# Kernel optimization log

Measured on AMD Instinct MI355X. Metric: run time of the kernel, lower is better.

## Reference

```python
import jax, jax.numpy as jnp
import numpy as np
from jax import lax


def setup_inputs() -> dict:
    key = jax.random.key(0)
    ks = jax.random.split(key, 6)
    B, L, Cin, N, Cout = 4, 4096, 256, 512, 256
    s = 0.02
    return {
        "x": jax.random.normal(ks[0], (B, L, Cin), dtype=jnp.float32),
        "Wx": jax.random.normal(ks[1], (Cin, N), dtype=jnp.float32) * s,
        "bx": jnp.zeros((N,), dtype=jnp.float32),
        "Wbc": jax.random.normal(ks[2], (Cin, 2 * N), dtype=jnp.float32) * s,
        "bbc": jnp.zeros((2 * N,), dtype=jnp.float32),
        "Wd": jax.random.normal(ks[3], (Cin, N), dtype=jnp.float32) * s,
        "bd": jnp.zeros((N,), dtype=jnp.float32),
        "Wy": jax.random.normal(ks[4], (N, Cout), dtype=jnp.float32) * s,
        "by": jnp.zeros((Cout,), dtype=jnp.float32),
    }


def _scan_combine(c1, c2):
    # linear recurrence h_t = a_t * h_{t-1} + b_t as an associative op
    a1, b1 = c1
    a2, b2 = c2
    return a1 * a2, a2 * b1 + b2


def reference(x, Wx, bx, Wbc, bbc, Wd, bd, Wy, by):
    # projections: [B, L, N]
    x_proj = x @ Wx + bx
    BC = x @ Wbc + bbc
    delta = x @ Wd + bd
    Bm, C = jnp.split(BC, 2, axis=-1)

    A_bar = jnp.exp(-jax.nn.softplus(delta))      # [B, L, N], in (0, 1)
    B_bar = (1.0 - A_bar) * Bm                    # [B, L, N]

    # selective scan (h0 = 0): h_t = A_bar_t * h_{t-1} + B_bar_t * x_proj_t
    u = B_bar * x_proj
    _, h = lax.associative_scan(_scan_combine, (A_bar, u), axis=1)

    y = C * h                                      # [B, L, N]
    return y @ Wy + by                             # [B, L, Cout]
```

## Files before the change

kernel.cpp:

```cpp
#include <hip/hip_runtime.h>
#include <math.h>

constexpr int CIN  = 256;
constexpr int NST  = 512;
constexpr int LSEQ = 4096;
constexpr int BB   = 4;
constexpr int ROWS = BB * LSEQ;
constexpr int COUT = 256;
constexpr int LC   = 32;
constexpr int NC   = LSEQ / LC;

typedef __attribute__((ext_vector_type(8))) short bf16x8;
typedef __attribute__((ext_vector_type(4))) float f32x4;
typedef unsigned short ushort_t;
typedef unsigned int   uint_t;

__device__ __forceinline__ ushort_t f2bf(float f) {
    uint_t u = __float_as_uint(f);
    u = (u + 0x7FFF + ((u >> 16) & 1)) >> 16;
    return (ushort_t)u;
}
__device__ __forceinline__ float bf2f(ushort_t s) {
    return __uint_as_float(((uint_t)s) << 16);
}

constexpr int WELEMS  = 4 * NST * CIN + COUT * NST;
constexpr int WBLOCKS = WELEMS / 256;
constexpr int XBLOCKS = (ROWS * CIN / 4) / 256;

__global__ __launch_bounds__(256)
void prep_kernel(const float* __restrict__ Wx, const float* __restrict__ Wbc,
                 const float* __restrict__ Wd, const float* __restrict__ Wy,
                 const float* __restrict__ x,
                 ushort_t* __restrict__ Wt, ushort_t* __restrict__ Wyt,
                 ushort_t* __restrict__ xb)
{
    const int bid = blockIdx.x;
    if (bid < WBLOCKS) {
        const int gid = bid * 256 + threadIdx.x;
        if (gid < 4 * NST * CIN) {
            const int mat = gid >> 17;
            const int idx = gid & 131071;
            const int k   = idx >> 9;
            const int n   = idx & 511;
            float v;
            if      (mat == 0) v = Wx [k * NST + n];
            else if (mat == 1) v = Wbc[k * (2 * NST) + n];
            else if (mat == 2) v = Wbc[k * (2 * NST) + NST + n];
            else               v = Wd [k * NST + n];
            Wt[((size_t)mat * NST + n) * CIN + k] = f2bf(v);
        } else {
            const int idx = gid - 4 * NST * CIN;
            const int k   = idx >> 8;
            const int n   = idx & 255;
            Wyt[(size_t)n * NST + k] = f2bf(Wy[k * COUT + n]);
        }
    } else {
        const int i = ((bid - WBLOCKS) * 256 + threadIdx.x) * 4;
        float4 v = *(const float4*)&x[i];
        uint2 o;
        o.x = (uint_t)f2bf(v.x) | ((uint_t)f2bf(v.y) << 16);
        o.y = (uint_t)f2bf(v.z) | ((uint_t)f2bf(v.w) << 16);
        *(uint2*)&xb[i] = o;
    }
}

__global__ __launch_bounds__(256, 3)
void proj_mfma_kernel(const ushort_t* __restrict__ xb, const ushort_t* __restrict__ Wt,
                      const float* __restrict__ bx, const float* __restrict__ bbc,
                      const float* __restrict__ bd,
                      float2* __restrict__ AU, ushort_t* __restrict__ CYb,
                      float* __restrict__ Aprod, float* __restrict__ Hend)
{
    __shared__ alignas(16) char smem[46080];
    ushort_t (*xs)[72]     = (ushort_t(*)[72])smem;
    ushort_t (*ws)[64][72] = (ushort_t(*)[64][72])(smem + 9216);
    float2   (*aus)[65]    = (float2(*)[65])smem;
    float2   (*comb)[64]   = (float2(*)[64])(smem + 33280);

    const int tid  = threadIdx.x;
    const int wave = tid >> 6;
    const int lane = tid & 63;
    const int lm   = lane & 15;
    const int lq   = lane >> 4;
    const int row0 = blockIdx.x * 64;
    const int n0   = blockIdx.y * 64;

    const int sr = tid >> 2;
    const int sk = (tid & 3) << 4;

    f32x4 acc[4][4];
    #pragma unroll
    for (int rt = 0; rt < 4; ++rt)
        #pragma unroll
        for (int m = 0; m < 4; ++m)
            acc[rt][m] = (f32x4){0.f, 0.f, 0.f, 0.f};

    const ushort_t* xsrc  = xb + (size_t)(row0 + sr) * CIN + sk;
    const ushort_t* wsrc0 = Wt + (size_t)(n0 + sr) * CIN + sk;

    for (int k0 = 0; k0 < CIN; k0 += 64) {
        uint4 xv0 = *(const uint4*)(xsrc + k0);
        uint4 xv1 = *(const uint4*)(xsrc + k0 + 8);
        uint4 wv[4][2];
        #pragma unroll
        for (int m = 0; m < 4; ++m) {
            const ushort_t* p = wsrc0 + (size_t)m * NST * CIN + k0;
            wv[m][0] = *(const uint4*)(p);
            wv[m][1] = *(const uint4*)(p + 8);
        }
        *(uint4*)&xs[sr][sk]     = xv0;
        *(uint4*)&xs[sr][sk + 8] = xv1;
        #pragma unroll
        for (int m = 0; m < 4; ++m) {
            *(uint4*)&ws[m][sr][sk]     = wv[m][0];
            *(uint4*)&ws[m][sr][sk + 8] = wv[m][1];
        }
        __syncthreads();

        #pragma unroll
        for (int ks = 0; ks < 2; ++ks) {
            const int kk = ks * 32 + lq * 8;
            bf16x8 af[4], bf[4];
            #pragma unroll
            for (int rt = 0; rt < 4; ++rt)
                af[rt] = *(const bf16x8*)&xs[rt * 16 + lm][kk];
            #pragma unroll
            for (int m = 0; m < 4; ++m)
                bf[m] = *(const bf16x8*)&ws[m][wave * 16 + lm][kk];
            #pragma unroll
            for (int rt = 0; rt < 4; ++rt)
                #pragma unroll
                for (int m = 0; m < 4; ++m)
                    acc[rt][m] = __builtin_amdgcn_mfma_f32_16x16x32_bf16(
                        af[rt], bf[m], acc[rt][m], 0, 0, 0);
        }
        __syncthreads();
    }

    const int nl = wave * 16 + lm;
    const int ng = n0 + nl;
    const float bxv = bx [ng];
    const float bbv = bbc[ng];
    const float bcv = bbc[NST + ng];
    const float bdv = bd [ng];
    #pragma unroll
    for (int rt = 0; rt < 4; ++rt) {
        #pragma unroll
        for (int r = 0; r < 4; ++r) {
            const int t   = rt * 16 + lq * 4 + r;
            const int row = row0 + t;
            float xp = acc[rt][0][r] + bxv;
            float bm = acc[rt][1][r] + bbv;
            float cc = acc[rt][2][r] + bcv;
            float dd = acc[rt][3][r] + bdv;
            dd = fminf(dd, 60.0f);
            float e  = __expf(dd);
            float A  = 1.0f / (1.0f + e);
            float u  = (e * A) * bm * xp;
            const size_t idx = (size_t)row * NST + ng;
            AU[idx]  = make_float2(A, u);
            CYb[idx] = f2bf(cc);
            aus[t][nl] = make_float2(A, u);
        }
    }
    __syncthreads();

    {
        const int n  = tid & 63;
        const int sg = tid >> 6;
        float ap = 1.0f, h = 0.0f;
        #pragma unroll
        for (int i = 0; i < 16; ++i) {
            float2 au = aus[sg * 16 + i][n];
            ap *= au.x;
            h  = fmaf(au.x, h, au.y);
        }
        comb[sg][n] = make_float2(ap, h);
    }
    __syncthreads();

    if (tid < 128) {
        const int n  = tid & 63;
        const int ch = tid >> 6;
        float2 c0 = comb[ch * 2 + 0][n];
        float2 c1 = comb[ch * 2 + 1][n];
        const size_t ci = (size_t)(blockIdx.x * 2 + ch) * NST + (n0 + n);
        Aprod[ci] = c0.x * c1.x;
        Hend[ci]  = fmaf(c1.x, c0.y, c1.y);
    }
}

__global__ __launch_bounds__(256)
void scan_carry_kernel(const float* __restrict__ Aprod, const float* __restrict__ Hend,
                       float* __restrict__ Carry)
{
    const int gid = blockIdx.x * 256 + threadIdx.x;
    const int n   = gid & (NST - 1);
    const int b   = gid >> 9;
    float h = 0.0f;
    for (int c = 0; c < NC; ++c) {
        size_t idx = ((size_t)(b * NC + c)) * NST + n;
        Carry[idx] = h;
        h = fmaf(Aprod[idx], h, Hend[idx]);
    }
}

__global__ __launch_bounds__(256)
void scan_final_kernel(const float2* __restrict__ AU, ushort_t* __restrict__ CYb,
                       const float* __restrict__ Carry)
{
    const int gid = blockIdx.x * 256 + threadIdx.x;
    const int n   = gid & (NST - 1);
    const int bc  = gid >> 9;
    const size_t base = (size_t)bc * LC * NST + n;
    float h = Carry[(size_t)bc * NST + n];
    #pragma unroll 8
    for (int t = 0; t < LC; ++t) {
        size_t idx = base + (size_t)t * NST;
        float2 au = AU[idx];
        float cc  = bf2f(CYb[idx]);
        h = fmaf(au.x, h, au.y);
        CYb[idx] = f2bf(cc * h);
    }
}

__global__ __launch_bounds__(256, 4)
void out_mfma_kernel(const ushort_t* __restrict__ yb, const ushort_t* __restrict__ Wyt,
                     const float* __restrict__ by, float* __restrict__ out)
{
    __shared__ alignas(16) ushort_t ys [64][72];
    __shared__ alignas(16) ushort_t wys[64][72];

    const int tid  = threadIdx.x;
    const int wave = tid >> 6;
    const int lane = tid & 63;
    const int lm   = lane & 15;
    const int lq   = lane >> 4;
    const int row0 = blockIdx.x * 64;
    const int n0   = blockIdx.y * 64;

    const int sr = tid >> 2;
    const int sk = (tid & 3) << 4;

    f32x4 acc[4];
    #pragma unroll
    for (int rt = 0; rt < 4; ++rt) acc[rt] = (f32x4){0.f, 0.f, 0.f, 0.f};

    const ushort_t* ysrc = yb  + (size_t)(row0 + sr) * NST + sk;
    const ushort_t* wsrc = Wyt + (size_t)(n0  + sr) * NST + sk;

    for (int k0 = 0; k0 < NST; k0 += 64) {
        uint4 yv0 = *(const uint4*)(ysrc + k0);
        uint4 yv1 = *(const uint4*)(ysrc + k0 + 8);
        uint4 wv0 = *(const uint4*)(wsrc + k0);
        uint4 wv1 = *(const uint4*)(wsrc + k0 + 8);
        *(uint4*)&ys [sr][sk]     = yv0;
        *(uint4*)&ys [sr][sk + 8] = yv1;
        *(uint4*)&wys[sr][sk]     = wv0;
        *(uint4*)&wys[sr][sk + 8] = wv1;
        __syncthreads();

        #pragma unroll
        for (int ks = 0; ks < 2; ++ks) {
            const int kk = ks * 32 + lq * 8;
            bf16x8 bfr = *(const bf16x8*)&wys[wave * 16 + lm][kk];
            #pragma unroll
            for (int rt = 0; rt < 4; ++rt) {
                bf16x8 af = *(const bf16x8*)&ys[rt * 16 + lm][kk];
                acc[rt] = __builtin_amdgcn_mfma_f32_16x16x32_bf16(
                    af, bfr, acc[rt], 0, 0, 0);
            }
        }
        __syncthreads();
    }

    const int ng = n0 + wave * 16 + lm;
    const float bv = by[ng];
    #pragma unroll
    for (int rt = 0; rt < 4; ++rt)
        #pragma unroll
        for (int r = 0; r < 4; ++r) {
            const int row = row0 + rt * 16 + lq * 4 + r;
            out[(size_t)row * COUT + ng] = acc[rt][r] + bv;
        }
}

extern "C" void kernel_launch(void* const* d_in, const int* in_sizes, int n_in,
                              void* d_out, int out_size, void* d_ws, size_t ws_size,
                              hipStream_t stream)
{
    const float* x   = (const float*)d_in[0];
    const float* Wx  = (const float*)d_in[1];
    const float* bx  = (const float*)d_in[2];
    const float* Wbc = (const float*)d_in[3];
    const float* bbc = (const float*)d_in[4];
    const float* Wd  = (const float*)d_in[5];
    const float* bd  = (const float*)d_in[6];
    const float* Wy  = (const float*)d_in[7];
    const float* by  = (const float*)d_in[8];
    float* out = (float*)d_out;

    char* p = (char*)d_ws;
    float2*   AU    = (float2*)p;         p += (size_t)ROWS * NST * 8;
    ushort_t* CYb   = (ushort_t*)p;       p += (size_t)ROWS * NST * 2;
    ushort_t* xb    = (ushort_t*)p;       p += (size_t)ROWS * CIN * 2;
    ushort_t* Wt    = (ushort_t*)p;       p += (size_t)4 * NST * CIN * 2;
    ushort_t* Wyt   = (ushort_t*)p;       p += (size_t)COUT * NST * 2;
    float*    Aprod = (float*)p;          p += (size_t)BB * NC * NST * 4;
    float*    Hend  = (float*)p;          p += (size_t)BB * NC * NST * 4;
    float*    Carry = (float*)p;          p += (size_t)BB * NC * NST * 4;

    prep_kernel<<<WBLOCKS + XBLOCKS, 256, 0, stream>>>(
        Wx, Wbc, Wd, Wy, x, Wt, Wyt, xb);

    proj_mfma_kernel<<<dim3(ROWS / 64, NST / 64), 256, 0, stream>>>(
        xb, Wt, bx, bbc, bd, AU, CYb, Aprod, Hend);

    scan_carry_kernel<<<(BB * NST) / 256, 256, 0, stream>>>(
        Aprod, Hend, Carry);

    scan_final_kernel<<<(BB * NC * NST) / 256, 256, 0, stream>>>(
        AU, CYb, Carry);

    out_mfma_kernel<<<dim3(ROWS / 64, COUT / 64), 256, 0, stream>>>(
        CYb, Wyt, by, out);
}
```

Before: 162.7 us.

## Store scan A/u as fp16, coalesce C stores, parallelize carry scan across waves

Packs the per-element decay A and input u into one half2 word written with nontemporal stores, halving the intermediate AU traffic between the projection and final scan kernels. The bf16 C values are staged in shared memory and written out as 16-byte vector stores. The chunk aggregates are merged into one float2 array. The serial carry loop over chunks is replaced by a wave-level shuffle scan, one wavefront per (batch, state) pair. The fp16 storage of A and u lowers precision of the recurrence inputs and may hurt accuracy for long sequences.

```diff
diff --git a/kernel.cpp b/kernel.cpp
--- a/kernel.cpp
+++ b/kernel.cpp
@@ -1,4 +1,5 @@
 #include <hip/hip_runtime.h>
+#include <hip/hip_fp16.h>
 #include <math.h>
 
 constexpr int CIN  = 256;
@@ -69,14 +70,15 @@
 void proj_mfma_kernel(const ushort_t* __restrict__ xb, const ushort_t* __restrict__ Wt,
                       const float* __restrict__ bx, const float* __restrict__ bbc,
                       const float* __restrict__ bd,
-                      float2* __restrict__ AU, ushort_t* __restrict__ CYb,
-                      float* __restrict__ Aprod, float* __restrict__ Hend)
+                      uint_t* __restrict__ AU, ushort_t* __restrict__ CYb,
+                      float2* __restrict__ AHc)
 {
     __shared__ alignas(16) char smem[46080];
     ushort_t (*xs)[72]     = (ushort_t(*)[72])smem;
     ushort_t (*ws)[64][72] = (ushort_t(*)[64][72])(smem + 9216);
     float2   (*aus)[65]    = (float2(*)[65])smem;
     float2   (*comb)[64]   = (float2(*)[64])(smem + 33280);
+    ushort_t (*cs)[72]     = (ushort_t(*)[72])(smem + 35328);
 
     const int tid  = threadIdx.x;
     const int wave = tid >> 6;
@@ -159,12 +161,23 @@
             float A  = 1.0f / (1.0f + e);
             float u  = (e * A) * bm * xp;
             const size_t idx = (size_t)row * NST + ng;
-            AU[idx]  = make_float2(A, u);
-            CYb[idx] = f2bf(cc);
+            __half2 hv = __floats2half2_rn(A, u);
+            __builtin_nontemporal_store(__builtin_bit_cast(uint_t, hv), &AU[idx]);
             aus[t][nl] = make_float2(A, u);
+            cs[t][nl]  = f2bf(cc);
         }
     }
     __syncthreads();
+
+    {
+        const int r  = tid >> 2;
+        const int ns = (tid & 3) << 4;
+        uint4 c0 = *(const uint4*)&cs[r][ns];
+        uint4 c1 = *(const uint4*)&cs[r][ns + 8];
+        ushort_t* dst = CYb + (size_t)(row0 + r) * NST + n0 + ns;
+        *(uint4*)dst       = c0;
+        *(uint4*)(dst + 8) = c1;
+    }
 
     {
         const int n  = tid & 63;
@@ -186,40 +199,65 @@
         float2 c0 = comb[ch * 2 + 0][n];
         float2 c1 = comb[ch * 2 + 1][n];
         const size_t ci = (size_t)(blockIdx.x * 2 + ch) * NST + (n0 + n);
-        Aprod[ci] = c0.x * c1.x;
-        Hend[ci]  = fmaf(c1.x, c0.y, c1.y);
+        AHc[ci] = make_float2(c0.x * c1.x, fmaf(c1.x, c0.y, c1.y));
     }
 }
 
 __global__ __launch_bounds__(256)
-void scan_carry_kernel(const float* __restrict__ Aprod, const float* __restrict__ Hend,
-                       float* __restrict__ Carry)
-{
-    const int gid = blockIdx.x * 256 + threadIdx.x;
-    const int n   = gid & (NST - 1);
-    const int b   = gid >> 9;
-    float h = 0.0f;
-    for (int c = 0; c < NC; ++c) {
-        size_t idx = ((size_t)(b * NC + c)) * NST + n;
-        Carry[idx] = h;
-        h = fmaf(Aprod[idx], h, Hend[idx]);
-    }
+void scan_carry_kernel(const float2* __restrict__ AHc, float* __restrict__ Carry2)
+{
+    const int wid  = (blockIdx.x * 256 + threadIdx.x) >> 6;
+    const int lane = threadIdx.x & 63;
+    const int b = wid >> 9;
+    const int n = wid & (NST - 1);
+
+    float2 v0 = AHc[(size_t)(b * NC + lane) * NST + n];
+    float a = v0.x, h = v0.y;
+    #pragma unroll
+    for (int d = 1; d < 64; d <<= 1) {
+        float ao = __shfl_up(a, d, 64);
+        float ho = __shfl_up(h, d, 64);
+        if (lane >= d) { h = fmaf(a, ho, h); a *= ao; }
+    }
+    float c0 = __shfl_up(h, 1, 64);
+    if (lane == 0) c0 = 0.0f;
+    const float Ht = __shfl(h, 63, 64);
+
+    float2 v1 = AHc[(size_t)(b * NC + 64 + lane) * NST + n];
+    float a1 = v1.x, h1 = v1.y;
+    #pragma unroll
+    for (int d = 1; d < 64; d <<= 1) {
+        float ao = __shfl_up(a1, d, 64);
+        float ho = __shfl_up(h1, d, 64);
+        if (lane >= d) { h1 = fmaf(a1, ho, h1); a1 *= ao; }
+    }
+    float pa = __shfl_up(a1, 1, 64);
+    float ph = __shfl_up(h1, 1, 64);
+    if (lane == 0) { pa = 1.0f; ph = 0.0f; }
+    float c1 = fmaf(pa, Ht, ph);
+
+    float* cp = Carry2 + (size_t)(b * NST + n) * NC;
+    cp[lane]      = c0;
+    cp[64 + lane] = c1;
 }
 
 __global__ __launch_bounds__(256)
-void scan_final_kernel(const float2* __restrict__ AU, ushort_t* __restrict__ CYb,
-                       const float* __restrict__ Carry)
+void scan_final_kernel(const uint_t* __restrict__ AU, ushort_t* __restrict__ CYb,
+                       const float* __restrict__ Carry2)
 {
     const int gid = blockIdx.x * 256 + threadIdx.x;
     const int n   = gid & (NST - 1);
     const int bc  = gid >> 9;
+    const int b   = bc >> 7;
+    const int c   = bc & (NC - 1);
     const size_t base = (size_t)bc * LC * NST + n;
-    float h = Carry[(size_t)bc * NST + n];
+    float h = Carry2[((size_t)b * NST + n) * NC + c];
     #pragma unroll 8
     for (int t = 0; t < LC; ++t) {
         size_t idx = base + (size_t)t * NST;
-        float2 au = AU[idx];
-        float cc  = bf2f(CYb[idx]);
+        uint_t raw = __builtin_nontemporal_load(&AU[idx]);
+        float2 au  = __half22float2(__builtin_bit_cast(__half2, raw));
+        float cc   = bf2f(CYb[idx]);
         h = fmaf(au.x, h, au.y);
         CYb[idx] = f2bf(cc * h);
     }
@@ -302,26 +340,24 @@
     float* out = (float*)d_out;
 
     char* p = (char*)d_ws;
-    float2*   AU    = (float2*)p;         p += (size_t)ROWS * NST * 8;
-    ushort_t* CYb   = (ushort_t*)p;       p += (size_t)ROWS * NST * 2;
-    ushort_t* xb    = (ushort_t*)p;       p += (size_t)ROWS * CIN * 2;
-    ushort_t* Wt    = (ushort_t*)p;       p += (size_t)4 * NST * CIN * 2;
-    ushort_t* Wyt   = (ushort_t*)p;       p += (size_t)COUT * NST * 2;
-    float*    Aprod = (float*)p;          p += (size_t)BB * NC * NST * 4;
-    float*    Hend  = (float*)p;          p += (size_t)BB * NC * NST * 4;
-    float*    Carry = (float*)p;          p += (size_t)BB * NC * NST * 4;
+    uint_t*   AU     = (uint_t*)p;        p += (size_t)ROWS * NST * 4;
+    ushort_t* CYb    = (ushort_t*)p;      p += (size_t)ROWS * NST * 2;
+    ushort_t* xb     = (ushort_t*)p;      p += (size_t)ROWS * CIN * 2;
+    ushort_t* Wt     = (ushort_t*)p;      p += (size_t)4 * NST * CIN * 2;
+    ushort_t* Wyt    = (ushort_t*)p;      p += (size_t)COUT * NST * 2;
+    float2*   AHc    = (float2*)p;        p += (size_t)BB * NC * NST * 8;
+    float*    Carry2 = (float*)p;         p += (size_t)BB * NST * NC * 4;
 
     prep_kernel<<<WBLOCKS + XBLOCKS, 256, 0, stream>>>(
         Wx, Wbc, Wd, Wy, x, Wt, Wyt, xb);
 
     proj_mfma_kernel<<<dim3(ROWS / 64, NST / 64), 256, 0, stream>>>(
-        xb, Wt, bx, bbc, bd, AU, CYb, Aprod, Hend);
-
-    scan_carry_kernel<<<(BB * NST) / 256, 256, 0, stream>>>(
-        Aprod, Hend, Carry);
+        xb, Wt, bx, bbc, bd, AU, CYb, AHc);
+
+    scan_carry_kernel<<<(BB * NST) / 4, 256, 0, stream>>>(AHc, Carry2);
 
     scan_final_kernel<<<(BB * NC * NST) / 256, 256, 0, stream>>>(
-        AU, CYb, Carry);
+        AU, CYb, Carry2);
 
     out_mfma_kernel<<<dim3(ROWS / 64, COUT / 64), 256, 0, stream>>>(
         CYb, Wyt, by, out);
```

New measurement: 147.8 us. -9.2%, faster.
